# Kernel optimization log

Hardware: AMD Instinct MI355X
Metric: run time of the kernel (lower is better)

## Reference

```python
import jax, jax.numpy as jnp
import numpy as np
from jax import lax

B, T, K = 32, 2048, 1024


def setup_inputs() -> dict:
    key = jax.random.key(0)
    x = jax.random.normal(key, (B, T, K), dtype=jnp.float32)
    return {"x": x}


def reference(x) -> jnp.ndarray:
    # x: [B, T, K]. Max-plus DP:
    #   out[:, 0]   = x[:, 0]
    #   out[:, i+1] = x[:, i+1] + max(out[:, i], shift_right(out[:, i], -inf))
    neg_inf = jnp.asarray(-jnp.inf, dtype=x.dtype)
    x_t = jnp.swapaxes(x, 0, 1)  # [T, B, K] time-major for scan

    def step(carry, xi):
        # carry: [B, K] = out row i; xi: [B, K] = x row i+1
        shifted = jnp.concatenate(
            [jnp.full_like(carry[:, :1], neg_inf), carry[:, :-1]], axis=1
        )
        new = xi + jnp.maximum(carry, shifted)
        return new, new

    init = x_t[0]
    _, rows = lax.scan(step, init, x_t[1:])  # rows: [T-1, B, K]
    out = jnp.concatenate([init[None], rows], axis=0)  # [T, B, K]
    return jnp.swapaxes(out, 0, 1)  # [B, T, K]
```

## Files before the change

### kernel.cpp

```cpp
#include <hip/hip_runtime.h>
#include <math.h>


#define BB 32
#define TT 2048
#define KK 1024
#define GG 8
#define WW (KK / GG)
#define RR 32
#define NT (TT / RR)
#define PD 8

typedef __attribute__((address_space(1))) void GV;
typedef __attribute__((address_space(3))) void LV;

__global__ __launch_bounds__(64, 1)
void harddtw_lds(const float* __restrict__ x, float* __restrict__ out,
                 int* __restrict__ flags, float* __restrict__ bws)
{
    const int bid  = blockIdx.x;
    const int g    = bid >> 5;
    const int b    = bid & 31;
    const int lane = threadIdx.x;
    const bool lz  = (lane == 0);

    const int k0 = g * WW;
    const int kc = k0 + (lane << 1);
    const size_t base = (size_t)b * TT * KK;

    float* ol = out + base + kc;

    int* myflag = flags + bid;
    int* upflag = flags + bid - 32;
    float*       mybw = bws + ((size_t)(b * GG + g)) * TT;
    const float* upbw = bws + ((size_t)(b * GG + g - 1)) * TT;

    __shared__ float lds[2][RR * WW];
    __shared__ float bsc[RR];

    const float* xstage = x + base + k0 + (size_t)(lane >> 5) * KK
                          + ((lane & 31) << 2);

    {
        const float* gp = xstage;
#pragma unroll
        for (int i = 0; i < RR / 2; ++i) {
            __builtin_amdgcn_global_load_lds((GV*)(void*)gp,
                                             (LV*)(void*)&lds[0][i * 256],
                                             16, 0, 0);
            gp += 2 * KK;
        }
    }

    float pv0 = 0.0f, pv1 = 0.0f;
    float sh_prev = 0.0f;
    float bcur = -INFINITY, bnxt = -INFINITY;

    if (g > 0) {
        while (__hip_atomic_load(upflag, __ATOMIC_RELAXED,
                                 __HIP_MEMORY_SCOPE_AGENT) < 1)
            __builtin_amdgcn_s_sleep(1);
        __asm__ volatile("" ::: "memory");
        if (lane == 0) {
            bcur = 0.0f;
        } else if (lane < RR) {
            bcur = __hip_atomic_load(upbw + lane - 1, __ATOMIC_RELAXED,
                                     __HIP_MEMORY_SCOPE_AGENT);
        }
    }

    __asm__ volatile("s_waitcnt vmcnt(0)" ::: "memory");

    float2 rb[PD];
    int buf = 0;
#pragma unroll
    for (int p = 0; p < PD; ++p)
        rb[p] = *(const float2*)&lds[0][p * WW + (lane << 1)];

#pragma unroll 1
    for (int r = 0; r < NT; ++r) {
        if (g > 0 && r < NT - 1) {
            while (__hip_atomic_load(upflag, __ATOMIC_RELAXED,
                                     __HIP_MEMORY_SCOPE_AGENT) < r + 2)
                __builtin_amdgcn_s_sleep(1);
            __asm__ volatile("" ::: "memory");
            if (lane < RR)
                bnxt = __hip_atomic_load(
                    upbw + (size_t)(r + 1) * RR + lane - 1,
                    __ATOMIC_RELAXED, __HIP_MEMORY_SCOPE_AGENT);
        }

        if (r < NT - 1) {
            const float* gp = xstage + (size_t)(r + 1) * RR * KK;
            float* lp = &lds[buf ^ 1][0];
#pragma unroll
            for (int i = 0; i < RR / 2; ++i) {
                __builtin_amdgcn_global_load_lds((GV*)(void*)gp,
                                                 (LV*)(void*)(lp + i * 256),
                                                 16, 0, 0);
                gp += 2 * KK;
            }
        }

        const bool pub = (g < GG - 1);

#pragma unroll
        for (int j = 0; j < RR; ++j) {
            float2 xv = rb[j & (PD - 1)];
            float bv = __int_as_float(
                __builtin_amdgcn_readlane(__float_as_int(bcur), j));
            float left = lz ? bv : sh_prev;
            float n0 = xv.x + fmaxf(pv0, left);
            float n1 = xv.y + fmaxf(pv1, pv0);
            float sh_new = __shfl_up(n1, 1);

            float2 o; o.x = n0; o.y = n1;
            *(float2*)ol = o;
            ol += KK;
            if (lane == 63) bsc[j] = n1;

            if (j < RR - PD)
                rb[j & (PD - 1)] =
                    *(const float2*)&lds[buf][(j + PD) * WW + (lane << 1)];

            pv0 = n0; pv1 = n1; sh_prev = sh_new;
            __builtin_amdgcn_sched_barrier(0);
        }

        bcur = bnxt;

        __asm__ volatile("s_waitcnt lgkmcnt(0)" ::: "memory");
        if (pub && lane < RR)
            __hip_atomic_store(mybw + (size_t)r * RR + lane, bsc[lane],
                               __ATOMIC_RELAXED, __HIP_MEMORY_SCOPE_AGENT);
        __asm__ volatile("s_waitcnt vmcnt(0)" ::: "memory");
        if (pub && lz)
            __hip_atomic_store(myflag, r + 1, __ATOMIC_RELAXED,
                               __HIP_MEMORY_SCOPE_AGENT);

        if (r < NT - 1) {
            buf ^= 1;
#pragma unroll
            for (int p = 0; p < PD; ++p)
                rb[p] = *(const float2*)&lds[buf][p * WW + (lane << 1)];
        }
    }
}

extern "C" void kernel_launch(void* const* d_in, const int* in_sizes, int n_in,
                              void* d_out, int out_size, void* d_ws, size_t ws_size,
                              hipStream_t stream) {
    (void)in_sizes; (void)n_in; (void)out_size; (void)ws_size;
    const float* x = (const float*)d_in[0];
    float* out = (float*)d_out;
    int* flags = (int*)d_ws;
    float* bws = (float*)((char*)d_ws + 4096);

    hipMemsetAsync(flags, 0, BB * GG * sizeof(int), stream);

    harddtw_lds<<<dim3(BB * GG), dim3(64), 0, stream>>>(x, out, flags, bws);
}
```

Measured before the change: 612.1 us.

## Bulk-load tile into registers and publish boundary column directly from lane 63

Replaces the 8-deep rolling LDS prefetch ring with a single bulk load of all 32 rows of the tile into registers before the serial row loop. It also removes the per-row sched_barrier and reorders each step to start the cross-lane shuffle early. Boundary values go straight from lane 63 to global memory as paired 64-bit atomic stores, instead of staging through shared memory and storing after an lgkmcnt wait. This shortens the dependent chain per row and drops the end-of-tile staging, at the cost of higher register pressure (64 floats per lane for the tile).

```diff
diff --git a/kernel.cpp b/kernel.cpp
--- a/kernel.cpp
+++ b/kernel.cpp
@@ -9,14 +9,13 @@
 #define WW (KK / GG)
 #define RR 32
 #define NT (TT / RR)
-#define PD 8
 
 typedef __attribute__((address_space(1))) void GV;
 typedef __attribute__((address_space(3))) void LV;
 
 __global__ __launch_bounds__(64, 1)
-void harddtw_lds(const float* __restrict__ x, float* __restrict__ out,
-                 int* __restrict__ flags, float* __restrict__ bws)
+void harddtw_td(const float* __restrict__ x, float* __restrict__ out,
+                int* __restrict__ flags, float* __restrict__ bws)
 {
     const int bid  = blockIdx.x;
     const int g    = bid >> 5;
@@ -36,7 +35,6 @@
     const float* upbw = bws + ((size_t)(b * GG + g - 1)) * TT;
 
     __shared__ float lds[2][RR * WW];
-    __shared__ float bsc[RR];
 
     const float* xstage = x + base + k0 + (size_t)(lane >> 5) * KK
                           + ((lane & 31) << 2);
@@ -71,11 +69,7 @@
 
     __asm__ volatile("s_waitcnt vmcnt(0)" ::: "memory");
 
-    float2 rb[PD];
     int buf = 0;
-#pragma unroll
-    for (int p = 0; p < PD; ++p)
-        rb[p] = *(const float2*)&lds[0][p * WW + (lane << 1)];
 
 #pragma unroll 1
     for (int r = 0; r < NT; ++r) {
@@ -102,48 +96,50 @@
             }
         }
 
+        float2 td[RR];
+#pragma unroll
+        for (int j = 0; j < RR; ++j)
+            td[j] = *(const float2*)&lds[buf][j * WW + (lane << 1)];
+        __builtin_amdgcn_sched_barrier(0);
+
         const bool pub = (g < GG - 1);
+        float bpair = 0.0f;
 
 #pragma unroll
         for (int j = 0; j < RR; ++j) {
-            float2 xv = rb[j & (PD - 1)];
+            float2 xv = td[j];
+            float n1 = xv.y + fmaxf(pv1, pv0);
+            float sh_new = __shfl_up(n1, 1);
             float bv = __int_as_float(
                 __builtin_amdgcn_readlane(__float_as_int(bcur), j));
             float left = lz ? bv : sh_prev;
             float n0 = xv.x + fmaxf(pv0, left);
-            float n1 = xv.y + fmaxf(pv1, pv0);
-            float sh_new = __shfl_up(n1, 1);
 
             float2 o; o.x = n0; o.y = n1;
             *(float2*)ol = o;
             ol += KK;
-            if (lane == 63) bsc[j] = n1;
 
-            if (j < RR - PD)
-                rb[j & (PD - 1)] =
-                    *(const float2*)&lds[buf][(j + PD) * WW + (lane << 1)];
+            if ((j & 1) == 0) {
+                bpair = n1;
+            } else if (pub && lane == 63) {
+                union { float f[2]; unsigned long long u; } cv;
+                cv.f[0] = bpair; cv.f[1] = n1;
+                __hip_atomic_store(
+                    (unsigned long long*)(mybw + (size_t)r * RR + (j - 1)),
+                    cv.u, __ATOMIC_RELAXED, __HIP_MEMORY_SCOPE_AGENT);
+            }
 
             pv0 = n0; pv1 = n1; sh_prev = sh_new;
-            __builtin_amdgcn_sched_barrier(0);
         }
 
         bcur = bnxt;
 
-        __asm__ volatile("s_waitcnt lgkmcnt(0)" ::: "memory");
-        if (pub && lane < RR)
-            __hip_atomic_store(mybw + (size_t)r * RR + lane, bsc[lane],
-                               __ATOMIC_RELAXED, __HIP_MEMORY_SCOPE_AGENT);
         __asm__ volatile("s_waitcnt vmcnt(0)" ::: "memory");
         if (pub && lz)
             __hip_atomic_store(myflag, r + 1, __ATOMIC_RELAXED,
                                __HIP_MEMORY_SCOPE_AGENT);
 
-        if (r < NT - 1) {
-            buf ^= 1;
-#pragma unroll
-            for (int p = 0; p < PD; ++p)
-                rb[p] = *(const float2*)&lds[buf][p * WW + (lane << 1)];
-        }
+        buf ^= 1;
     }
 }
 
@@ -158,5 +154,5 @@
 
     hipMemsetAsync(flags, 0, BB * GG * sizeof(int), stream);
 
-    harddtw_lds<<<dim3(BB * GG), dim3(64), 0, stream>>>(x, out, flags, bws);
+    harddtw_td<<<dim3(BB * GG), dim3(64), 0, stream>>>(x, out, flags, bws);
 }
```

Result: faster. 598.3 us (-2.2%).
